# Kernel tuning notes

Measured on AMD Instinct MI355X. Metric: run time of the kernel, lower is better.

The kernel has to match this reference:

```python
import jax, jax.numpy as jnp
import numpy as np
from jax import lax

DIM = 256
PROJ = 128
NPOS = 8          # ceil(log2(2*64+5))
EXT = 64          # attnExtension
NLAYERS = 4
HEADS = 4
KDIM = PROJ + NPOS
EPS = 1e-5


def _ln(x):
    # LayerNorm over last dim, no affine (elementwise_affine=False)
    mu = jnp.mean(x, axis=-1, keepdims=True)
    var = jnp.mean(jnp.square(x - mu), axis=-1, keepdims=True)
    return (x - mu) * lax.rsqrt(var + EPS)


def setup_inputs() -> dict:
    key = jax.random.key(0)
    ks = jax.random.split(key, 18)
    L = 2048
    s = 0.05
    return {
        "input": jax.random.normal(ks[0], (L, PROJ), jnp.float32),
        "residual": jax.random.normal(ks[1], (5 * L, DIM), jnp.float32),
        "W_proj": jax.random.normal(ks[2], (5 * DIM, KDIM), jnp.float32) * s,
        "b_proj": jnp.zeros((5 * DIM,), jnp.float32),
        "Wq": jax.random.normal(ks[3], (DIM, DIM), jnp.float32) * s,
        "bq": jnp.zeros((DIM,), jnp.float32),
        "Wk": jax.random.normal(ks[4], (DIM, KDIM), jnp.float32) * s,
        "bk": jnp.zeros((DIM,), jnp.float32),
        "Wv": jax.random.normal(ks[5], (DIM, KDIM), jnp.float32) * s,
        "bv": jnp.zeros((DIM,), jnp.float32),
        "Wo": jax.random.normal(ks[6], (DIM, DIM), jnp.float32) * s,
        "bo": jnp.zeros((DIM,), jnp.float32),
        "conv_w": jax.random.normal(ks[7], (NLAYERS, DIM, DIM, 3), jnp.float32) * s,
        "conv_b": jnp.zeros((NLAYERS, DIM), jnp.float32),
        "W_skip": jax.random.normal(ks[8], (DIM, DIM), jnp.float32) * s,
        "b_skip": jnp.zeros((DIM,), jnp.float32),
    }


def reference(input, residual, W_proj, b_proj, Wq, bq, Wk, bk, Wv, bv,
              Wo, bo, conv_w, conv_b, W_skip, b_skip):
    L = input.shape[0]
    T = 5 * L  # tgt length
    hd = DIM // HEADS

    # positional embeddings: pos[:, i] = (arange(L) % 2^(i+1)) / 2^i
    n = jnp.arange(L, dtype=input.dtype)[:, None]
    i = jnp.arange(NPOS, dtype=input.dtype)[None, :]
    pos = jnp.mod(n, 2.0 ** (i + 1.0)) / (2.0 ** i)

    src = jnp.concatenate([input, pos], axis=1)            # (L, KDIM)
    tgt = (src @ W_proj.T + b_proj).reshape(T, DIM)        # (5L, DIM)

    # banded mask: row j may attend col i iff 5i-EXT <= j < 5i+5+EXT
    j = jnp.arange(T)[:, None]
    ii = jnp.arange(L)[None, :]
    d = j - 5 * ii
    allowed = (d >= -EXT) & (d < 5 + EXT)                  # (5L, L)

    # multihead attention (eval mode, dropout skipped)
    q = (tgt @ Wq.T + bq).reshape(T, HEADS, hd).transpose(1, 0, 2)
    k = (src @ Wk.T + bk).reshape(L, HEADS, hd).transpose(1, 0, 2)
    v = (src @ Wv.T + bv).reshape(L, HEADS, hd).transpose(1, 0, 2)
    scores = jnp.einsum('hqd,hkd->hqk', q, k) / jnp.sqrt(jnp.asarray(hd, q.dtype))
    scores = jnp.where(allowed[None], scores, -jnp.inf)
    attn = jax.nn.softmax(scores, axis=-1)
    ctx = jnp.einsum('hqk,hkd->hqd', attn, v).transpose(1, 0, 2).reshape(T, DIM)
    attn_out = ctx @ Wo.T + bo

    cnn_in = _ln(attn_out) + residual                      # (5L, DIM)

    # spectral-norm conv stack (weights assumed pre-normalized) + tanh
    x = cnn_in.T[None]                                     # (1, DIM, 5L)
    for l in range(NLAYERS):
        x = jnp.tanh(
            lax.conv_general_dilated(x, conv_w[l], window_strides=(1,),
                                     padding=[(1, 1)])
            + conv_b[l][None, :, None])
    cnn_out = x[0].T                                       # (5L, DIM)

    return _ln(cnn_out + cnn_in @ W_skip.T + b_skip)
```

## Files before the change

### kernel.cpp

```cpp
#include <hip/hip_runtime.h>
#include <hip/hip_bf16.h>

#define PROJ 128
#define KPAD 192
#define EPS 1e-5f
#define CVALID 40

typedef __attribute__((ext_vector_type(4))) float f32x4;
typedef __attribute__((ext_vector_type(8))) short bf16x8;
typedef __attribute__((ext_vector_type(4))) unsigned int u32x4;

__device__ inline float bflo(unsigned u){ union{unsigned x;float f;}c; c.x = u<<16; return c.f; }
__device__ inline float bfhi(unsigned u){ union{unsigned x;float f;}c; c.x = u & 0xffff0000u; return c.f; }
__device__ inline float bf2f(unsigned short u){ union{unsigned x;float f;}c; c.x = ((unsigned)u)<<16; return c.f; }
__device__ inline unsigned short f2bf(float f){
    union{float f; unsigned u;} c; c.f = f;
    unsigned r = c.u + 0x7fff + ((c.u >> 16) & 1);
    return (unsigned short)(r >> 16);
}
__device__ __forceinline__ bf16x8 asbf(u32x4 u){ union{u32x4 a; bf16x8 b;} c; c.a = u; return c.b; }
__device__ __forceinline__ unsigned pk2(float a, float b){
    return (unsigned)f2bf(a) | ((unsigned)f2bf(b) << 16);
}

__global__ __launch_bounds__(256) void prep_all(
    const float* __restrict__ W_proj, const float* __restrict__ Wq,
    const float* __restrict__ Wk, const float* __restrict__ Wv,
    const float* __restrict__ Wo, const float* __restrict__ Ws,
    const float* __restrict__ convw, const float* __restrict__ input,
    const float* __restrict__ bq, const float* __restrict__ b_proj,
    unsigned short* __restrict__ Wqb, unsigned short* __restrict__ Wkb,
    unsigned short* __restrict__ Wvb, unsigned short* __restrict__ Wob,
    unsigned short* __restrict__ Wsb, unsigned short* __restrict__ Wcb,
    unsigned short* __restrict__ WpbT, unsigned short* __restrict__ srcb,
    float* __restrict__ zbias, float* __restrict__ bqc, int L)
{
    int idx = blockIdx.x * 256 + threadIdx.x;
    if (idx < 81920) {
        int w = idx >> 6, lanei = idx & 63;
        int r = w >> 8, o = w & 255;
        const float* wrow = Wq + (size_t)o * 256;
        const float* bp = b_proj + r * 256;
        float s = 0.f;
        #pragma unroll
        for (int c = 0; c < 256; c += 64) s += wrow[c + lanei] * bp[c + lanei];
        #pragma unroll
        for (int m = 32; m > 0; m >>= 1) s += __shfl_xor(s, m, 64);
        if (lanei == 0) bqc[w] = s + bq[o];
        return;
    }
    idx -= 81920;
    if (idx < 8192) {
        const float* s = Wq + (size_t)idx * 8;
        *(u32x4*)&Wqb[(size_t)idx * 8] =
            (u32x4){pk2(s[0],s[1]), pk2(s[2],s[3]), pk2(s[4],s[5]), pk2(s[6],s[7])};
        return;
    }
    idx -= 8192;
    if (idx < 12288) {
        int which = idx / 6144, t = idx % 6144;
        int r = t / 24, c0 = (t % 24) * 8;
        const float* W = which ? Wv : Wk;
        unsigned short* D = which ? Wvb : Wkb;
        u32x4 v = {0,0,0,0};
        if (c0 < 136) {
            const float* s = W + (size_t)r * 136 + c0;
            v = (u32x4){pk2(s[0],s[1]), pk2(s[2],s[3]), pk2(s[4],s[5]), pk2(s[6],s[7])};
        }
        *(u32x4*)&D[(size_t)r * 192 + c0] = v;
        return;
    }
    idx -= 12288;
    if (idx < 16384) {
        int which = idx / 8192, t = idx % 8192;
        int lane = t & 63, fr = (t >> 6) & 3, wid = (t >> 8) & 7, kt = t >> 11;
        int o = wid * 32 + (fr >> 1) * 16 + (lane & 15);
        int c = kt * 64 + (fr & 1) * 32 + (lane >> 4) * 8;
        const float* s = (which ? Ws : Wo) + (size_t)o * 256 + c;
        unsigned short* D = which ? Wsb : Wob;
        *(u32x4*)&D[(size_t)t * 8] =
            (u32x4){pk2(s[0],s[1]), pk2(s[2],s[3]), pk2(s[4],s[5]), pk2(s[6],s[7])};
        return;
    }
    idx -= 16384;
    if (idx < 98304) {
        int t = idx;
        int lane = t & 63, fr = (t >> 6) & 3, wid = (t >> 8) & 7, ktl = t >> 11;
        int l = ktl / 12, kt = ktl % 12;
        int o = wid * 32 + (fr >> 1) * 16 + (lane & 15);
        int c = kt * 64 + (fr & 1) * 32 + (lane >> 4) * 8;
        int ktap = c >> 8, ci = c & 255;
        const float* s = convw + (((size_t)l * 256 + o) * 256 + ci) * 3 + ktap;
        float v[8];
        #pragma unroll
        for (int j = 0; j < 8; ++j) v[j] = s[(size_t)j * 3];
        *(u32x4*)&Wcb[(size_t)t * 8] =
            (u32x4){pk2(v[0],v[1]), pk2(v[2],v[3]), pk2(v[4],v[5]), pk2(v[6],v[7])};
        return;
    }
    idx -= 98304;
    if (idx < 40960) {
        int t = idx;
        int r = t >> 13;
        int c = (t >> 5) & 255;
        int d0 = (t & 31) * 8;
        u32x4 v = {0,0,0,0};
        if (c < 136) {
            const float* s = W_proj + ((size_t)(r * 256 + d0)) * 136 + c;
            float x[8];
            #pragma unroll
            for (int j = 0; j < 8; ++j) x[j] = s[(size_t)j * 136];
            v = (u32x4){pk2(x[0],x[1]), pk2(x[2],x[3]), pk2(x[4],x[5]), pk2(x[6],x[7])};
        }
        *(u32x4*)&WpbT[(size_t)t * 8] = v;
        return;
    }
    idx -= 40960;
    if (idx < L * 24) {
        int n = idx / 24, c0 = (idx % 24) * 8;
        u32x4 v = {0,0,0,0};
        if (c0 < PROJ) {
            const float* s = input + (size_t)n * PROJ + c0;
            v = (u32x4){pk2(s[0],s[1]), pk2(s[2],s[3]), pk2(s[4],s[5]), pk2(s[6],s[7])};
        } else if (c0 == PROJ) {
            float p[8];
            #pragma unroll
            for (int i = 0; i < 8; ++i) {
                int mask = (2 << i) - 1;
                p[i] = (float)(n & mask) / (float)(1 << i);
            }
            v = (u32x4){pk2(p[0],p[1]), pk2(p[2],p[3]), pk2(p[4],p[5]), pk2(p[6],p[7])};
        }
        *(u32x4*)&srcb[(size_t)n * KPAD + c0] = v;
        return;
    }
    idx -= L * 24;
    if (idx < 256) { zbias[idx] = 0.f; return; }
}

__device__ __forceinline__ void gemm_core_64x128(
    unsigned short (&As)[64][72], unsigned short (&Bs)[128][72],
    const unsigned short* __restrict__ A, int lda,
    const unsigned short* __restrict__ B, int ldb,
    const float* __restrict__ bias,
    unsigned short* __restrict__ C, int ldc,
    int K, int m0, int n0)
{
    const int tid = threadIdx.x;
    const int lane = tid & 63;
    const int wid = tid >> 6;
    const int wm = wid >> 1, wn = wid & 1;

    const int ar = tid >> 2, asg = tid & 3;
    const int br = tid >> 1, bsg = tid & 1;

    const unsigned short* Ap = A + (size_t)(m0 + ar) * lda + asg * 16;
    const unsigned short* Bp = B + (size_t)(n0 + br) * ldb + bsg * 32;

    u32x4 ra0, ra1, rb0, rb1, rb2, rb3;
    auto loadregs = [&](int k0) {
        ra0 = *(const u32x4*)(Ap + k0);
        ra1 = *(const u32x4*)(Ap + k0 + 8);
        rb0 = *(const u32x4*)(Bp + k0);
        rb1 = *(const u32x4*)(Bp + k0 + 8);
        rb2 = *(const u32x4*)(Bp + k0 + 16);
        rb3 = *(const u32x4*)(Bp + k0 + 24);
    };
    auto stlds = [&]() {
        *(u32x4*)&As[ar][asg * 16]      = ra0;
        *(u32x4*)&As[ar][asg * 16 + 8]  = ra1;
        *(u32x4*)&Bs[br][bsg * 32]      = rb0;
        *(u32x4*)&Bs[br][bsg * 32 + 8]  = rb1;
        *(u32x4*)&Bs[br][bsg * 32 + 16] = rb2;
        *(u32x4*)&Bs[br][bsg * 32 + 24] = rb3;
    };

    f32x4 acc[2][4];
    #pragma unroll
    for (int i = 0; i < 2; ++i)
        #pragma unroll
        for (int j = 0; j < 4; ++j) acc[i][j] = (f32x4){0.f, 0.f, 0.f, 0.f};

    loadregs(0);
    stlds();
    __syncthreads();

    const int rowf = lane & 15, kb = lane >> 4;
    const int ktiles = K >> 6;
    for (int kt = 0; kt < ktiles; ++kt) {
        if (kt + 1 < ktiles) loadregs((kt + 1) << 6);
        #pragma unroll
        for (int ks = 0; ks < 2; ++ks) {
            bf16x8 af[2], bfr[4];
            #pragma unroll
            for (int i = 0; i < 2; ++i)
                af[i] = *(const bf16x8*)&As[wm * 32 + i * 16 + rowf][ks * 32 + kb * 8];
            #pragma unroll
            for (int j = 0; j < 4; ++j)
                bfr[j] = *(const bf16x8*)&Bs[wn * 64 + j * 16 + rowf][ks * 32 + kb * 8];
            #pragma unroll
            for (int i = 0; i < 2; ++i)
                #pragma unroll
                for (int j = 0; j < 4; ++j)
                    acc[i][j] = __builtin_amdgcn_mfma_f32_16x16x32_bf16(af[i], bfr[j], acc[i][j], 0, 0, 0);
        }
        __syncthreads();
        if (kt + 1 < ktiles) { stlds(); __syncthreads(); }
    }

    const int rq = lane >> 4;
    #pragma unroll
    for (int i = 0; i < 2; ++i) {
        int gm = m0 + wm * 32 + i * 16 + rq * 4;
        #pragma unroll
        for (int j = 0; j < 4; ++j) {
            int gn = n0 + wn * 64 + j * 16 + rowf;
            float bv = bias[gn];
            #pragma unroll
            for (int r = 0; r < 4; ++r)
                C[(size_t)(gm + r) * ldc + gn] = f2bf(acc[i][j][r] + bv);
        }
    }
}

__global__ __launch_bounds__(256) void combine_wq(
    const unsigned short* __restrict__ Wqb,
    const unsigned short* __restrict__ WpbT,
    const float* __restrict__ zbias,
    unsigned short* __restrict__ Wqpb)
{
    __shared__ unsigned short As[64][72];
    __shared__ unsigned short Bs[128][72];
    int bi = blockIdx.x;
    int r = bi >> 3, rem = bi & 7;
    int m0 = (rem >> 1) * 64, n0 = (rem & 1) * 128;
    gemm_core_64x128(As, Bs, Wqb, 256, WpbT + (size_t)r * 65536, 256, zbias,
                     Wqpb + (size_t)r * 65536, 256, 256, m0, n0);
}

__global__ __launch_bounds__(256) void qkv_fused(
    const unsigned short* __restrict__ srcb,
    const unsigned short* __restrict__ Wqpb,
    const unsigned short* __restrict__ Wkb,
    const unsigned short* __restrict__ Wvb,
    const float* __restrict__ bqc, const float* __restrict__ bk,
    const float* __restrict__ bv,
    unsigned short* __restrict__ qb, unsigned short* __restrict__ kb,
    unsigned short* __restrict__ vb)
{
    __shared__ unsigned short As[64][72];
    __shared__ unsigned short Bs[128][72];
    int bi = blockIdx.x;
    const unsigned short *B;
    const float* bias;
    unsigned short* C;
    int ldb, K, m0, n0, ldc;
    if (bi < 320) {
        B = Wqpb; bias = bqc; C = qb; ldb = 256; K = 192; ldc = 1280;
        m0 = (bi / 10) * 64; n0 = (bi % 10) * 128;
    } else if (bi < 384) {
        int t = bi - 320;
        B = Wkb; bias = bk; C = kb; ldb = 192; K = 192; ldc = 256;
        m0 = (t >> 1) * 64; n0 = (t & 1) * 128;
    } else {
        int t = bi - 384;
        B = Wvb; bias = bv; C = vb; ldb = 192; K = 192; ldc = 256;
        m0 = (t >> 1) * 64; n0 = (t & 1) * 128;
    }
    gemm_core_64x128(As, Bs, srcb, KPAD, B, ldb, bias, C, ldc, K, m0, n0);
}

__global__ __launch_bounds__(256) void attn16(
    const unsigned short* __restrict__ q,
    const unsigned short* __restrict__ k,
    const unsigned short* __restrict__ v,
    unsigned short* __restrict__ ctx, int L)
{
    __shared__ unsigned short ksm[30][264];
    __shared__ unsigned short vsm[30][264];
    const int j0 = blockIdx.x * 16;
    const int iblk0 = (j0 >= 68) ? (j0 - 64) / 5 : 0;
    int ihim = (j0 + 79) / 5; if (ihim > L - 1) ihim = L - 1;
    const int NR = ihim - iblk0 + 1;

    for (int e = threadIdx.x; e < 30 * 32; e += 256) {
        int rr = e >> 5, cc = (e & 31) * 8;
        u32x4 kz = {0, 0, 0, 0}, vz = {0, 0, 0, 0};
        if (rr < NR) {
            kz = *(const u32x4*)&k[(size_t)(iblk0 + rr) * 256 + cc];
            vz = *(const u32x4*)&v[(size_t)(iblk0 + rr) * 256 + cc];
        }
        *(u32x4*)&ksm[rr][cc] = kz;
        *(u32x4*)&vsm[rr][cc] = vz;
    }
    __syncthreads();

    const int tid = threadIdx.x;
    const int h = tid >> 6, lane = tid & 63;
    const int qq = lane & 15, p = lane >> 4;
    const int j = j0 + qq;
    const int colb = h * 64 + p * 16;

    float qr[16];
    {
        u32x4 q0 = *(const u32x4*)&q[(size_t)j * 256 + colb];
        u32x4 q1 = *(const u32x4*)&q[(size_t)j * 256 + colb + 8];
        #pragma unroll
        for (int w = 0; w < 4; ++w) {
            qr[2 * w]     = bflo(q0[w]) * 0.125f;
            qr[2 * w + 1] = bfhi(q0[w]) * 0.125f;
            qr[8 + 2 * w]     = bflo(q1[w]) * 0.125f;
            qr[8 + 2 * w + 1] = bfhi(q1[w]) * 0.125f;
        }
    }
    const int ilo = (j >= 68) ? (j - 64) / 5 : 0;
    int ihi = (j + 64) / 5; if (ihi > L - 1) ihi = L - 1;

    float sc[30];
    #pragma unroll
    for (int t = 0; t < 30; ++t) {
        int i = iblk0 + t;
        u32x4 k0 = *(const u32x4*)&ksm[t][colb];
        u32x4 k1 = *(const u32x4*)&ksm[t][colb + 8];
        float s = 0.f;
        #pragma unroll
        for (int w = 0; w < 4; ++w) {
            s += qr[2 * w]     * bflo(k0[w]);
            s += qr[2 * w + 1] * bfhi(k0[w]);
            s += qr[8 + 2 * w]     * bflo(k1[w]);
            s += qr[8 + 2 * w + 1] * bfhi(k1[w]);
        }
        s += __shfl_xor(s, 16, 64);
        s += __shfl_xor(s, 32, 64);
        sc[t] = (i >= ilo && i <= ihi) ? s : -1e30f;
    }
    float mx = -1e30f;
    #pragma unroll
    for (int t = 0; t < 30; ++t) mx = fmaxf(mx, sc[t]);
    float den = 0.f, o[16];
    #pragma unroll
    for (int d = 0; d < 16; ++d) o[d] = 0.f;
    #pragma unroll
    for (int t = 0; t < 30; ++t) {
        float pt = __expf(sc[t] - mx);
        den += pt;
        u32x4 v0 = *(const u32x4*)&vsm[t][colb];
        u32x4 v1 = *(const u32x4*)&vsm[t][colb + 8];
        #pragma unroll
        for (int w = 0; w < 4; ++w) {
            o[2 * w]     += pt * bflo(v0[w]);
            o[2 * w + 1] += pt * bfhi(v0[w]);
            o[8 + 2 * w]     += pt * bflo(v1[w]);
            o[8 + 2 * w + 1] += pt * bfhi(v1[w]);
        }
    }
    float inv = 1.f / den;
    #pragma unroll
    for (int d = 0; d < 16; ++d)
        ctx[(size_t)j * 256 + colb + d] = f2bf(o[d] * inv);
}

__device__ __forceinline__ void wload4a(u32x4 (&b)[4], const unsigned short* p) {
    asm volatile(
        "global_load_dwordx4 %0, %4, off\n\t"
        "global_load_dwordx4 %1, %4, off offset:1024\n\t"
        "global_load_dwordx4 %2, %4, off offset:2048\n\t"
        "global_load_dwordx4 %3, %4, off offset:3072"
        : "=&v"(b[0]), "=&v"(b[1]), "=&v"(b[2]), "=&v"(b[3])
        : "v"(p));
}
__device__ __forceinline__ void wwait8a(u32x4 (&b)[4]) {
    asm volatile("s_waitcnt vmcnt(8)" : "+v"(b[0]), "+v"(b[1]), "+v"(b[2]), "+v"(b[3]));
}
__device__ __forceinline__ void wwait4a(u32x4 (&b)[4]) {
    asm volatile("s_waitcnt vmcnt(4)" : "+v"(b[0]), "+v"(b[1]), "+v"(b[2]), "+v"(b[3]));
}
__device__ __forceinline__ void wwait0a(u32x4 (&b)[4]) {
    asm volatile("s_waitcnt vmcnt(0)" : "+v"(b[0]), "+v"(b[1]), "+v"(b[2]), "+v"(b[3]));
}

template<int NKT, int DTMODE, int NROW>
__device__ __forceinline__ void frag_gemm(
    const unsigned short* __restrict__ Wp,
    const unsigned short (*actin)[264],
    f32x4 (&acc)[NROW][2], int wid, int lane)
{
    const int rowf = lane & 15, kq = lane >> 4;
    const unsigned short* base = Wp + wid * 2048 + lane * 8;
    u32x4 W[3][4];

    wload4a(W[0], base);
    if (NKT > 1) wload4a(W[1], base + 16384);
    if (NKT > 2) wload4a(W[2], base + 2 * 16384);
    if (NKT > 2)      wwait8a(W[0]);
    else if (NKT > 1) wwait4a(W[0]);
    else              wwait0a(W[0]);

    #pragma unroll
    for (int kt = 0; kt < NKT; ++kt) {
        u32x4 (&cur)[4] = W[kt % 3];
        const int dt = (DTMODE == 0) ? (kt >> 2) : (DTMODE == 1 ? 1 : 0);
        const int cb = (DTMODE == 0) ? ((kt & 3) * 64) : (kt * 64);
        #pragma unroll
        for (int ks = 0; ks < 2; ++ks) {
            bf16x8 w0 = asbf(ks ? cur[1] : cur[0]);
            bf16x8 w1 = asbf(ks ? cur[3] : cur[2]);
            #pragma unroll
            for (int i = 0; i < NROW; ++i) {
                bf16x8 a = *(const bf16x8*)&actin[i * 16 + rowf + dt][cb + ks * 32 + kq * 8];
                acc[i][0] = __builtin_amdgcn_mfma_f32_16x16x32_bf16(a, w0, acc[i][0], 0, 0, 0);
                acc[i][1] = __builtin_amdgcn_mfma_f32_16x16x32_bf16(a, w1, acc[i][1], 0, 0, 0);
            }
        }
        if (kt + 3 < NKT) {
            wload4a(cur, base + (size_t)(kt + 3) * 16384);
            wwait8a(W[(kt + 1) % 3]);
        } else if (kt + 2 < NKT) {
            wwait4a(W[(kt + 1) % 3]);
        } else if (kt + 1 < NKT) {
            wwait0a(W[(kt + 1) % 3]);
        }
    }
}

__global__ __launch_bounds__(512)
__attribute__((amdgpu_waves_per_eu(2)))
void conv_mega(
    const unsigned short* __restrict__ ctx,
    const float* __restrict__ residual,
    const unsigned short* __restrict__ Wob,
    const float* __restrict__ bo,
    const unsigned short* __restrict__ Wcb,
    const float* __restrict__ conv_b,
    const unsigned short* __restrict__ Wsb,
    const float* __restrict__ b_skip,
    float* __restrict__ out, int T)
{
    __shared__ unsigned short actA[50][264];
    __shared__ unsigned short actB[64][264];
    __shared__ float redS[64][8];
    __shared__ float redQ[64][8];

    const int tid = threadIdx.x;
    const int lane = tid & 63;
    const int wid = tid >> 6;
    const int rowf = lane & 15;
    const int kq = lane >> 4;
    const int t0 = blockIdx.x * CVALID;
    const int gn0 = wid * 32 + rowf;

    for (int e = tid; e < 64 * 32; e += 512) {
        int b = e >> 5, c = (e & 31) * 8;
        int g = t0 - 5 + b;
        u32x4 z = {0, 0, 0, 0};
        if (g >= 0 && g < T)
            z = *(const u32x4*)&ctx[(size_t)g * 256 + c];
        *(u32x4*)&actB[b][c] = z;
    }
    __syncthreads();

    f32x4 wacc[4][2];
    #pragma unroll
    for (int i = 0; i < 4; ++i)
        #pragma unroll
        for (int j = 0; j < 2; ++j) wacc[i][j] = (f32x4){0.f, 0.f, 0.f, 0.f};
    frag_gemm<4, 2, 4>(Wob, actB, wacc, wid, lane);

    float bo0 = bo[gn0], bo1 = bo[gn0 + 16];
    #pragma unroll
    for (int i = 0; i < 4; ++i)
        #pragma unroll
        for (int r = 0; r < 4; ++r) {
            float a = wacc[i][0][r] + bo0;
            float b = wacc[i][1][r] + bo1;
            wacc[i][0][r] = a; wacc[i][1][r] = b;
            float s = a + b;
            float q = a * a + b * b;
            #pragma unroll
            for (int m = 1; m < 16; m <<= 1) {
                s += __shfl_xor(s, m, 64);
                q += __shfl_xor(q, m, 64);
            }
            if (rowf == 0) {
                int row = i * 16 + kq * 4 + r;
                redS[row][wid] = s;
                redQ[row][wid] = q;
            }
        }
    __syncthreads();

    #pragma unroll
    for (int i = 0; i < 4; ++i)
        #pragma unroll
        for (int r = 0; r < 4; ++r) {
            int row = i * 16 + kq * 4 + r;
            if (row >= 50) continue;
            int g = t0 - 5 + row;
            float s = 0.f, q = 0.f;
            #pragma unroll
            for (int x = 0; x < 8; ++x) { s += redS[row][x]; q += redQ[row][x]; }
            float mu = s * (1.f / 256.f);
            float var = q * (1.f / 256.f) - mu * mu;
            float rs = rsqrtf(var + EPS);
            unsigned short o0 = 0, o1 = 0;
            if (g >= 0 && g < T) {
                o0 = f2bf((wacc[i][0][r] - mu) * rs + residual[(size_t)g * 256 + gn0]);
                o1 = f2bf((wacc[i][1][r] - mu) * rs + residual[(size_t)g * 256 + gn0 + 16]);
            }
            actA[row][gn0]      = o0;
            actA[row][gn0 + 16] = o1;
        }
    __syncthreads();

    f32x4 skipacc[3][2];
    #pragma unroll
    for (int i = 0; i < 3; ++i)
        #pragma unroll
        for (int j = 0; j < 2; ++j) skipacc[i][j] = (f32x4){0.f, 0.f, 0.f, 0.f};
    frag_gemm<4, 1, 3>(Wsb, actA, skipacc, wid, lane);

    f32x4 cacc[3][2];
    #pragma unroll 1
    for (int l2 = 0; l2 < 2; ++l2) {
        const int le = 2 * l2;
        #pragma unroll
        for (int i = 0; i < 3; ++i)
            #pragma unroll
            for (int j = 0; j < 2; ++j) cacc[i][j] = (f32x4){0.f, 0.f, 0.f, 0.f};
        frag_gemm<12, 0, 3>(Wcb + (size_t)le * 196608, actA, cacc, wid, lane);
        {
            float b0 = conv_b[le * 256 + gn0];
            float b1 = conv_b[le * 256 + gn0 + 16];
            #pragma unroll
            for (int i = 0; i < 3; ++i)
                #pragma unroll
                for (int r = 0; r < 4; ++r) {
                    int w = i * 16 + kq * 4 + r;
                    int g = t0 - 4 + w;
                    bool ok = (g >= 0 && g < T);
                    float v0 = cacc[i][0][r] + b0;
                    float v1 = cacc[i][1][r] + b1;
                    v0 = 1.f - 2.f / (__expf(2.f * v0) + 1.f);
                    v1 = 1.f - 2.f / (__expf(2.f * v1) + 1.f);
                    actB[w + 1][gn0]      = ok ? f2bf(v0) : (unsigned short)0;
                    actB[w + 1][gn0 + 16] = ok ? f2bf(v1) : (unsigned short)0;
                }
            if (tid < 256) actB[0][tid] = 0; else actB[49][tid - 256] = 0;
            __syncthreads();
        }

        const int lo = 2 * l2 + 1;
        #pragma unroll
        for (int i = 0; i < 3; ++i)
            #pragma unroll
            for (int j = 0; j < 2; ++j) cacc[i][j] = (f32x4){0.f, 0.f, 0.f, 0.f};
        frag_gemm<12, 0, 3>(Wcb + (size_t)lo * 196608, actB, cacc, wid, lane);
        {
            float b0 = conv_b[lo * 256 + gn0];
            float b1 = conv_b[lo * 256 + gn0 + 16];
            if (l2 == 0) {
                #pragma unroll
                for (int i = 0; i < 3; ++i)
                    #pragma unroll
                    for (int r = 0; r < 4; ++r) {
                        int w = i * 16 + kq * 4 + r;
                        int g = t0 - 4 + w;
                        bool ok = (g >= 0 && g < T);
                        float v0 = cacc[i][0][r] + b0;
                        float v1 = cacc[i][1][r] + b1;
                        v0 = 1.f - 2.f / (__expf(2.f * v0) + 1.f);
                        v1 = 1.f - 2.f / (__expf(2.f * v1) + 1.f);
                        actA[w + 1][gn0]      = ok ? f2bf(v0) : (unsigned short)0;
                        actA[w + 1][gn0 + 16] = ok ? f2bf(v1) : (unsigned short)0;
                    }
                if (tid < 256) actA[0][tid] = 0; else actA[49][tid - 256] = 0;
                __syncthreads();
            } else {
                float sb0 = b_skip[gn0], sb1 = b_skip[gn0 + 16];
                #pragma unroll
                for (int i = 0; i < 3; ++i)
                    #pragma unroll
                    for (int r = 0; r < 4; ++r) {
                        int w = i * 16 + kq * 4 + r;
                        int g = t0 - 4 + w;
                        bool ok = (g >= 0 && g < T);
                        float v0 = cacc[i][0][r] + b0;
                        float v1 = cacc[i][1][r] + b1;
                        v0 = ok ? (1.f - 2.f / (__expf(2.f * v0) + 1.f)) : 0.f;
                        v1 = ok ? (1.f - 2.f / (__expf(2.f * v1) + 1.f)) : 0.f;
                        skipacc[i][0][r] += sb0 + v0;
                        skipacc[i][1][r] += sb1 + v1;
                    }
            }
        }
    }

    #pragma unroll
    for (int i = 0; i < 3; ++i)
        #pragma unroll
        for (int r = 0; r < 4; ++r) {
            float a = skipacc[i][0][r], b = skipacc[i][1][r];
            float s = a + b;
            float q = a * a + b * b;
            #pragma unroll
            for (int m = 1; m < 16; m <<= 1) {
                s += __shfl_xor(s, m, 64);
                q += __shfl_xor(q, m, 64);
            }
            if (rowf == 0) {
                int row = i * 16 + kq * 4 + r;
                redS[row][wid] = s;
                redQ[row][wid] = q;
            }
        }
    __syncthreads();

    #pragma unroll
    for (int i = 0; i < 3; ++i)
        #pragma unroll
        for (int r = 0; r < 4; ++r) {
            int row = i * 16 + kq * 4 + r;
            if (row < 4 || row >= 44) continue;
            int g = t0 - 4 + row;
            if (g >= T) continue;
            float s = 0.f, q = 0.f;
            #pragma unroll
            for (int x = 0; x < 8; ++x) { s += redS[row][x]; q += redQ[row][x]; }
            float mu = s * (1.f / 256.f);
            float var = q * (1.f / 256.f) - mu * mu;
            float rs = rsqrtf(var + EPS);
            out[(size_t)g * 256 + gn0]      = (skipacc[i][0][r] - mu) * rs;
            out[(size_t)g * 256 + gn0 + 16] = (skipacc[i][1][r] - mu) * rs;
        }
}

extern "C" void kernel_launch(void* const* d_in, const int* in_sizes, int n_in,
                              void* d_out, int out_size, void* d_ws, size_t ws_size,
                              hipStream_t stream) {
    const float* input    = (const float*)d_in[0];
    const float* residual = (const float*)d_in[1];
    const float* W_proj   = (const float*)d_in[2];
    const float* b_proj   = (const float*)d_in[3];
    const float* Wq       = (const float*)d_in[4];
    const float* bq       = (const float*)d_in[5];
    const float* Wk       = (const float*)d_in[6];
    const float* bk       = (const float*)d_in[7];
    const float* Wv       = (const float*)d_in[8];
    const float* bv       = (const float*)d_in[9];
    const float* Wo       = (const float*)d_in[10];
    const float* bo       = (const float*)d_in[11];
    const float* conv_w   = (const float*)d_in[12];
    const float* conv_b   = (const float*)d_in[13];
    const float* W_skip   = (const float*)d_in[14];
    const float* b_skip   = (const float*)d_in[15];
    float* out = (float*)d_out;

    const int L = in_sizes[0] / PROJ;
    const int T = 5 * L;

    unsigned short* w16 = (unsigned short*)d_ws;
    size_t off = 0;
    auto alloc = [&](size_t n) { unsigned short* p = w16 + off; off += n; return p; };
    unsigned short* Wqb   = alloc(65536);
    unsigned short* Wkb   = alloc(49152);
    unsigned short* Wvb   = alloc(49152);
    unsigned short* Wob   = alloc(65536);
    unsigned short* Wsb   = alloc(65536);
    unsigned short* Wcb   = alloc(786432);
    unsigned short* WpbT  = alloc(327680);
    unsigned short* Wqpb  = alloc(327680);
    unsigned short* srcb  = alloc((size_t)L * KPAD);
    unsigned short* tgtb  = alloc((size_t)T * 256);
    unsigned short* qb    = alloc((size_t)T * 256);
    unsigned short* kb    = alloc((size_t)L * 256);
    unsigned short* vb    = alloc((size_t)L * 256);
    float* zbias = (float*)alloc(512);
    float* bqc   = (float*)alloc(2560);

    prep_all<<<dim3(1201), 256, 0, stream>>>(
        W_proj, Wq, Wk, Wv, Wo, W_skip, conv_w, input, bq, b_proj,
        Wqb, Wkb, Wvb, Wob, Wsb, Wcb, WpbT, srcb, zbias, bqc, L);

    combine_wq<<<dim3(40), 256, 0, stream>>>(Wqb, WpbT, zbias, Wqpb);

    qkv_fused<<<dim3(448), 256, 0, stream>>>(
        srcb, Wqpb, Wkb, Wvb, bqc, bk, bv, qb, kb, vb);

    attn16<<<dim3(T / 16), 256, 0, stream>>>(qb, kb, vb, tgtb, L);

    conv_mega<<<dim3(T / CVALID), 512, 0, stream>>>(
        tgtb, residual, Wob, bo, Wcb, conv_b, Wsb, b_skip, out, T);
}
```

Measured before the change: 85.16 us.

## Split conv_mega across 16 waves with one 16-column MFMA tile each

The fused conv/skip/LN kernel now launches 1024 threads (16 waves), each owning a single 16-output-column tile instead of two, and the weight pre-packing layout is changed to match. Residual loads and the first Wo weight prefetch are issued before the activation staging barrier so they overlap it, and shared memory moves to dynamic allocation with 16-way reduction buffers. The aim is more latency hiding and MFMA parallelism per block. In exchange, each wave re-reads the activation fragments for half as much work, and LDS traffic and register pressure per block rise.

```diff
diff --git a/kernel.cpp b/kernel.cpp
--- a/kernel.cpp
+++ b/kernel.cpp
@@ -73,9 +73,12 @@
     idx -= 12288;
     if (idx < 16384) {
         int which = idx / 8192, t = idx % 8192;
-        int lane = t & 63, fr = (t >> 6) & 3, wid = (t >> 8) & 7, kt = t >> 11;
-        int o = wid * 32 + (fr >> 1) * 16 + (lane & 15);
-        int c = kt * 64 + (fr & 1) * 32 + (lane >> 4) * 8;
+        int lane = t & 63;
+        int ks = (t >> 6) & 1;
+        int wid = (t >> 7) & 15;
+        int kt = t >> 11;
+        int o = wid * 16 + (lane & 15);
+        int c = kt * 64 + ks * 32 + (lane >> 4) * 8;
         const float* s = (which ? Ws : Wo) + (size_t)o * 256 + c;
         unsigned short* D = which ? Wsb : Wob;
         *(u32x4*)&D[(size_t)t * 8] =
@@ -85,10 +88,13 @@
     idx -= 16384;
     if (idx < 98304) {
         int t = idx;
-        int lane = t & 63, fr = (t >> 6) & 3, wid = (t >> 8) & 7, ktl = t >> 11;
+        int lane = t & 63;
+        int ks = (t >> 6) & 1;
+        int wid = (t >> 7) & 15;
+        int ktl = t >> 11;
         int l = ktl / 12, kt = ktl % 12;
-        int o = wid * 32 + (fr >> 1) * 16 + (lane & 15);
-        int c = kt * 64 + (fr & 1) * 32 + (lane >> 4) * 8;
+        int o = wid * 16 + (lane & 15);
+        int c = kt * 64 + ks * 32 + (lane >> 4) * 8;
         int ktap = c >> 8, ci = c & 255;
         const float* s = convw + (((size_t)l * 256 + o) * 256 + ci) * 3 + ktap;
         float v[8];
@@ -360,71 +366,74 @@
         ctx[(size_t)j * 256 + colb + d] = f2bf(o[d] * inv);
 }
 
-__device__ __forceinline__ void wload4a(u32x4 (&b)[4], const unsigned short* p) {
+__device__ __forceinline__ void wload2a(u32x4 (&b)[2], const unsigned short* p) {
     asm volatile(
-        "global_load_dwordx4 %0, %4, off\n\t"
-        "global_load_dwordx4 %1, %4, off offset:1024\n\t"
-        "global_load_dwordx4 %2, %4, off offset:2048\n\t"
-        "global_load_dwordx4 %3, %4, off offset:3072"
-        : "=&v"(b[0]), "=&v"(b[1]), "=&v"(b[2]), "=&v"(b[3])
-        : "v"(p));
-}
-__device__ __forceinline__ void wwait8a(u32x4 (&b)[4]) {
-    asm volatile("s_waitcnt vmcnt(8)" : "+v"(b[0]), "+v"(b[1]), "+v"(b[2]), "+v"(b[3]));
-}
-__device__ __forceinline__ void wwait4a(u32x4 (&b)[4]) {
-    asm volatile("s_waitcnt vmcnt(4)" : "+v"(b[0]), "+v"(b[1]), "+v"(b[2]), "+v"(b[3]));
-}
-__device__ __forceinline__ void wwait0a(u32x4 (&b)[4]) {
-    asm volatile("s_waitcnt vmcnt(0)" : "+v"(b[0]), "+v"(b[1]), "+v"(b[2]), "+v"(b[3]));
+        "global_load_dwordx4 %0, %2, off\n\t"
+        "global_load_dwordx4 %1, %2, off offset:1024"
+        : "=&v"(b[0]), "=&v"(b[1]) : "v"(p));
+}
+__device__ __forceinline__ void w2wait4(u32x4 (&b)[2]) {
+    asm volatile("s_waitcnt vmcnt(4)" : "+v"(b[0]), "+v"(b[1]));
+}
+__device__ __forceinline__ void w2wait2(u32x4 (&b)[2]) {
+    asm volatile("s_waitcnt vmcnt(2)" : "+v"(b[0]), "+v"(b[1]));
+}
+__device__ __forceinline__ void w2wait0(u32x4 (&b)[2]) {
+    asm volatile("s_waitcnt vmcnt(0)" : "+v"(b[0]), "+v"(b[1]));
 }
 
 template<int NKT, int DTMODE, int NROW>
-__device__ __forceinline__ void frag_gemm(
+__device__ __forceinline__ void frag_gemm16_body(
+    const unsigned short* __restrict__ base,
+    const unsigned short (*actin)[264],
+    f32x4 (&acc)[NROW], u32x4 (&W)[3][2], int lane)
+{
+    const int rowf = lane & 15, kq = lane >> 4;
+    if (NKT > 2)      w2wait4(W[0]);
+    else if (NKT > 1) w2wait2(W[0]);
+    else              w2wait0(W[0]);
+
+    #pragma unroll
+    for (int kt = 0; kt < NKT; ++kt) {
+        u32x4 (&cur)[2] = W[kt % 3];
+        const int dt = (DTMODE == 0) ? (kt >> 2) : (DTMODE == 1 ? 1 : 0);
+        const int cb = (DTMODE == 0) ? ((kt & 3) * 64) : (kt * 64);
+        #pragma unroll
+        for (int ks = 0; ks < 2; ++ks) {
+            bf16x8 w = asbf(cur[ks]);
+            #pragma unroll
+            for (int i = 0; i < NROW; ++i) {
+                bf16x8 a = *(const bf16x8*)&actin[i * 16 + rowf + dt][cb + ks * 32 + kq * 8];
+                acc[i] = __builtin_amdgcn_mfma_f32_16x16x32_bf16(a, w, acc[i], 0, 0, 0);
+            }
+        }
+        if (kt + 3 < NKT) {
+            wload2a(cur, base + (size_t)(kt + 3) * 16384);
+            w2wait4(W[(kt + 1) % 3]);
+        } else if (kt + 2 < NKT) {
+            w2wait2(W[(kt + 1) % 3]);
+        } else if (kt + 1 < NKT) {
+            w2wait0(W[(kt + 1) % 3]);
+        }
+    }
+}
+
+template<int NKT, int DTMODE, int NROW>
+__device__ __forceinline__ void frag_gemm16(
     const unsigned short* __restrict__ Wp,
     const unsigned short (*actin)[264],
-    f32x4 (&acc)[NROW][2], int wid, int lane)
+    f32x4 (&acc)[NROW], int wid, int lane)
 {
-    const int rowf = lane & 15, kq = lane >> 4;
-    const unsigned short* base = Wp + wid * 2048 + lane * 8;
-    u32x4 W[3][4];
-
-    wload4a(W[0], base);
-    if (NKT > 1) wload4a(W[1], base + 16384);
-    if (NKT > 2) wload4a(W[2], base + 2 * 16384);
-    if (NKT > 2)      wwait8a(W[0]);
-    else if (NKT > 1) wwait4a(W[0]);
-    else              wwait0a(W[0]);
-
-    #pragma unroll
-    for (int kt = 0; kt < NKT; ++kt) {
-        u32x4 (&cur)[4] = W[kt % 3];
-        const int dt = (DTMODE == 0) ? (kt >> 2) : (DTMODE == 1 ? 1 : 0);
-        const int cb = (DTMODE == 0) ? ((kt & 3) * 64) : (kt * 64);
-        #pragma unroll
-        for (int ks = 0; ks < 2; ++ks) {
-            bf16x8 w0 = asbf(ks ? cur[1] : cur[0]);
-            bf16x8 w1 = asbf(ks ? cur[3] : cur[2]);
-            #pragma unroll
-            for (int i = 0; i < NROW; ++i) {
-                bf16x8 a = *(const bf16x8*)&actin[i * 16 + rowf + dt][cb + ks * 32 + kq * 8];
-                acc[i][0] = __builtin_amdgcn_mfma_f32_16x16x32_bf16(a, w0, acc[i][0], 0, 0, 0);
-                acc[i][1] = __builtin_amdgcn_mfma_f32_16x16x32_bf16(a, w1, acc[i][1], 0, 0, 0);
-            }
-        }
-        if (kt + 3 < NKT) {
-            wload4a(cur, base + (size_t)(kt + 3) * 16384);
-            wwait8a(W[(kt + 1) % 3]);
-        } else if (kt + 2 < NKT) {
-            wwait4a(W[(kt + 1) % 3]);
-        } else if (kt + 1 < NKT) {
-            wwait0a(W[(kt + 1) % 3]);
-        }
-    }
-}
-
-__global__ __launch_bounds__(512)
-__attribute__((amdgpu_waves_per_eu(2)))
+    const unsigned short* base = Wp + wid * 1024 + lane * 8;
+    u32x4 W[3][2];
+    wload2a(W[0], base);
+    if (NKT > 1) wload2a(W[1], base + 16384);
+    if (NKT > 2) wload2a(W[2], base + 2 * 16384);
+    frag_gemm16_body<NKT, DTMODE, NROW>(base, actin, acc, W, lane);
+}
+
+__global__ __launch_bounds__(1024)
+__attribute__((amdgpu_waves_per_eu(4)))
 void conv_mega(
     const unsigned short* __restrict__ ctx,
     const float* __restrict__ residual,
@@ -436,10 +445,12 @@
     const float* __restrict__ b_skip,
     float* __restrict__ out, int T)
 {
-    __shared__ unsigned short actA[50][264];
-    __shared__ unsigned short actB[64][264];
-    __shared__ float redS[64][8];
-    __shared__ float redQ[64][8];
+    extern __shared__ char smem[];
+    typedef unsigned short u16;
+    u16 (*actA)[264] = (u16(*)[264])smem;
+    u16 (*actB)[264] = (u16(*)[264])(smem + 26400);
+    float (*redS)[16] = (float(*)[16])(smem + 60192);
+    float (*redQ)[16] = (float(*)[16])(smem + 64288);
 
     const int tid = threadIdx.x;
     const int lane = tid & 63;
@@ -447,9 +458,30 @@
     const int rowf = lane & 15;
     const int kq = lane >> 4;
     const int t0 = blockIdx.x * CVALID;
-    const int gn0 = wid * 32 + rowf;
-
-    for (int e = tid; e < 64 * 32; e += 512) {
+    const int gn0 = wid * 16 + rowf;
+
+    float resv[4][4];
+    #pragma unroll
+    for (int i = 0; i < 4; ++i)
+        #pragma unroll
+        for (int r = 0; r < 4; ++r) {
+            int row = i * 16 + kq * 4 + r;
+            int g = t0 - 5 + row;
+            float r0 = 0.f;
+            if (row < 50 && g >= 0 && g < T) {
+                const float* p = residual + (size_t)g * 256 + gn0;
+                asm volatile("global_load_dword %0, %1, off" : "=&v"(r0) : "v"(p));
+            }
+            resv[i][r] = r0;
+        }
+
+    const unsigned short* wbase0 = Wob + wid * 1024 + lane * 8;
+    u32x4 WW[3][2];
+    wload2a(WW[0], wbase0);
+    wload2a(WW[1], wbase0 + 16384);
+    wload2a(WW[2], wbase0 + 2 * 16384);
+
+    for (int e = tid; e < 64 * 32; e += 1024) {
         int b = e >> 5, c = (e & 31) * 8;
         int g = t0 - 5 + b;
         u32x4 z = {0, 0, 0, 0};
@@ -459,23 +491,20 @@
     }
     __syncthreads();
 
-    f32x4 wacc[4][2];
+    f32x4 wacc[4];
+    #pragma unroll
+    for (int i = 0; i < 4; ++i) wacc[i] = (f32x4){0.f, 0.f, 0.f, 0.f};
+    frag_gemm16_body<4, 2, 4>(wbase0, actB, wacc, WW, lane);
+
+    float bo0 = bo[gn0];
     #pragma unroll
     for (int i = 0; i < 4; ++i)
         #pragma unroll
-        for (int j = 0; j < 2; ++j) wacc[i][j] = (f32x4){0.f, 0.f, 0.f, 0.f};
-    frag_gemm<4, 2, 4>(Wob, actB, wacc, wid, lane);
-
-    float bo0 = bo[gn0], bo1 = bo[gn0 + 16];
-    #pragma unroll
-    for (int i = 0; i < 4; ++i)
-        #pragma unroll
         for (int r = 0; r < 4; ++r) {
-            float a = wacc[i][0][r] + bo0;
-            float b = wacc[i][1][r] + bo1;
-            wacc[i][0][r] = a; wacc[i][1][r] = b;
-            float s = a + b;
-            float q = a * a + b * b;
+            float a = wacc[i][r] + bo0;
+            wacc[i][r] = a;
+            float s = a;
+            float q = a * a;
             #pragma unroll
             for (int m = 1; m < 16; m <<= 1) {
                 s += __shfl_xor(s, m, 64);
@@ -489,6 +518,12 @@
         }
     __syncthreads();
 
+    asm volatile("s_waitcnt vmcnt(0)");
+    #pragma unroll
+    for (int i = 0; i < 4; ++i)
+        asm volatile("" : "+v"(resv[i][0]), "+v"(resv[i][1]),
+                          "+v"(resv[i][2]), "+v"(resv[i][3]));
+
     #pragma unroll
     for (int i = 0; i < 4; ++i)
         #pragma unroll
@@ -498,39 +533,31 @@
             int g = t0 - 5 + row;
             float s = 0.f, q = 0.f;
             #pragma unroll
-            for (int x = 0; x < 8; ++x) { s += redS[row][x]; q += redQ[row][x]; }
+            for (int x = 0; x < 16; ++x) { s += redS[row][x]; q += redQ[row][x]; }
             float mu = s * (1.f / 256.f);
             float var = q * (1.f / 256.f) - mu * mu;
             float rs = rsqrtf(var + EPS);
-            unsigned short o0 = 0, o1 = 0;
-            if (g >= 0 && g < T) {
-                o0 = f2bf((wacc[i][0][r] - mu) * rs + residual[(size_t)g * 256 + gn0]);
-                o1 = f2bf((wacc[i][1][r] - mu) * rs + residual[(size_t)g * 256 + gn0 + 16]);
-            }
-            actA[row][gn0]      = o0;
-            actA[row][gn0 + 16] = o1;
+            unsigned short o0 = 0;
+            if (g >= 0 && g < T)
+                o0 = f2bf((wacc[i][r] - mu) * rs + resv[i][r]);
+            actA[row][gn0] = o0;
         }
     __syncthreads();
 
-    f32x4 skipacc[3][2];
-    #pragma unroll
-    for (int i = 0; i < 3; ++i)
-        #pragma unroll
-        for (int j = 0; j < 2; ++j) skipacc[i][j] = (f32x4){0.f, 0.f, 0.f, 0.f};
-    frag_gemm<4, 1, 3>(Wsb, actA, skipacc, wid, lane);
-
-    f32x4 cacc[3][2];
+    f32x4 skipacc[3];
+    #pragma unroll
+    for (int i = 0; i < 3; ++i) skipacc[i] = (f32x4){0.f, 0.f, 0.f, 0.f};
+    frag_gemm16<4, 1, 3>(Wsb, actA, skipacc, wid, lane);
+
+    f32x4 cacc[3];
     #pragma unroll 1
     for (int l2 = 0; l2 < 2; ++l2) {
         const int le = 2 * l2;
         #pragma unroll
-        for (int i = 0; i < 3; ++i)
-            #pragma unroll
-            for (int j = 0; j < 2; ++j) cacc[i][j] = (f32x4){0.f, 0.f, 0.f, 0.f};
-        frag_gemm<12, 0, 3>(Wcb + (size_t)le * 196608, actA, cacc, wid, lane);
+        for (int i = 0; i < 3; ++i) cacc[i] = (f32x4){0.f, 0.f, 0.f, 0.f};
+        frag_gemm16<12, 0, 3>(Wcb + (size_t)le * 196608, actA, cacc, wid, lane);
         {
             float b0 = conv_b[le * 256 + gn0];
-            float b1 = conv_b[le * 256 + gn0 + 16];
             #pragma unroll
             for (int i = 0; i < 3; ++i)
                 #pragma unroll
@@ -538,26 +565,21 @@
                     int w = i * 16 + kq * 4 + r;
                     int g = t0 - 4 + w;
                     bool ok = (g >= 0 && g < T);
-                    float v0 = cacc[i][0][r] + b0;
-                    float v1 = cacc[i][1][r] + b1;
+                    float v0 = cacc[i][r] + b0;
                     v0 = 1.f - 2.f / (__expf(2.f * v0) + 1.f);
-                    v1 = 1.f - 2.f / (__expf(2.f * v1) + 1.f);
-                    actB[w + 1][gn0]      = ok ? f2bf(v0) : (unsigned short)0;
-                    actB[w + 1][gn0 + 16] = ok ? f2bf(v1) : (unsigned short)0;
+                    actB[w + 1][gn0] = ok ? f2bf(v0) : (unsigned short)0;
                 }
-            if (tid < 256) actB[0][tid] = 0; else actB[49][tid - 256] = 0;
+            if (tid < 256) actB[0][tid] = 0;
+            else if (tid < 512) actB[49][tid - 256] = 0;
             __syncthreads();
         }
 
         const int lo = 2 * l2 + 1;
         #pragma unroll
-        for (int i = 0; i < 3; ++i)
-            #pragma unroll
-            for (int j = 0; j < 2; ++j) cacc[i][j] = (f32x4){0.f, 0.f, 0.f, 0.f};
-        frag_gemm<12, 0, 3>(Wcb + (size_t)lo * 196608, actB, cacc, wid, lane);
+        for (int i = 0; i < 3; ++i) cacc[i] = (f32x4){0.f, 0.f, 0.f, 0.f};
+        frag_gemm16<12, 0, 3>(Wcb + (size_t)lo * 196608, actB, cacc, wid, lane);
         {
             float b0 = conv_b[lo * 256 + gn0];
-            float b1 = conv_b[lo * 256 + gn0 + 16];
             if (l2 == 0) {
                 #pragma unroll
                 for (int i = 0; i < 3; ++i)
@@ -566,17 +588,15 @@
                         int w = i * 16 + kq * 4 + r;
                         int g = t0 - 4 + w;
                         bool ok = (g >= 0 && g < T);
-                        float v0 = cacc[i][0][r] + b0;
-                        float v1 = cacc[i][1][r] + b1;
+                        float v0 = cacc[i][r] + b0;
                         v0 = 1.f - 2.f / (__expf(2.f * v0) + 1.f);
-                        v1 = 1.f - 2.f / (__expf(2.f * v1) + 1.f);
-                        actA[w + 1][gn0]      = ok ? f2bf(v0) : (unsigned short)0;
-                        actA[w + 1][gn0 + 16] = ok ? f2bf(v1) : (unsigned short)0;
+                        actA[w + 1][gn0] = ok ? f2bf(v0) : (unsigned short)0;
                     }
-                if (tid < 256) actA[0][tid] = 0; else actA[49][tid - 256] = 0;
+                if (tid < 256) actA[0][tid] = 0;
+                else if (tid < 512) actA[49][tid - 256] = 0;
                 __syncthreads();
             } else {
-                float sb0 = b_skip[gn0], sb1 = b_skip[gn0 + 16];
+                float sb0 = b_skip[gn0];
                 #pragma unroll
                 for (int i = 0; i < 3; ++i)
                     #pragma unroll
@@ -584,12 +604,9 @@
                         int w = i * 16 + kq * 4 + r;
                         int g = t0 - 4 + w;
                         bool ok = (g >= 0 && g < T);
-                        float v0 = cacc[i][0][r] + b0;
-                        float v1 = cacc[i][1][r] + b1;
+                        float v0 = cacc[i][r] + b0;
                         v0 = ok ? (1.f - 2.f / (__expf(2.f * v0) + 1.f)) : 0.f;
-                        v1 = ok ? (1.f - 2.f / (__expf(2.f * v1) + 1.f)) : 0.f;
-                        skipacc[i][0][r] += sb0 + v0;
-                        skipacc[i][1][r] += sb1 + v1;
+                        skipacc[i][r] += sb0 + v0;
                     }
             }
         }
@@ -599,9 +616,9 @@
     for (int i = 0; i < 3; ++i)
         #pragma unroll
         for (int r = 0; r < 4; ++r) {
-            float a = skipacc[i][0][r], b = skipacc[i][1][r];
-            float s = a + b;
-            float q = a * a + b * b;
+            float a = skipacc[i][r];
+            float s = a;
+            float q = a * a;
             #pragma unroll
             for (int m = 1; m < 16; m <<= 1) {
                 s += __shfl_xor(s, m, 64);
@@ -625,12 +642,11 @@
             if (g >= T) continue;
             float s = 0.f, q = 0.f;
             #pragma unroll
-            for (int x = 0; x < 8; ++x) { s += redS[row][x]; q += redQ[row][x]; }
+            for (int x = 0; x < 16; ++x) { s += redS[row][x]; q += redQ[row][x]; }
             float mu = s * (1.f / 256.f);
             float var = q * (1.f / 256.f) - mu * mu;
             float rs = rsqrtf(var + EPS);
-            out[(size_t)g * 256 + gn0]      = (skipacc[i][0][r] - mu) * rs;
-            out[(size_t)g * 256 + gn0 + 16] = (skipacc[i][1][r] - mu) * rs;
+            out[(size_t)g * 256 + gn0] = (skipacc[i][r] - mu) * rs;
         }
 }
 
@@ -688,6 +704,8 @@
 
     attn16<<<dim3(T / 16), 256, 0, stream>>>(qb, kb, vb, tgtb, L);
 
-    conv_mega<<<dim3(T / CVALID), 512, 0, stream>>>(
+    hipFuncSetAttribute((const void*)conv_mega,
+                        hipFuncAttributeMaxDynamicSharedMemorySize, 69632);
+    conv_mega<<<dim3(T / CVALID), 1024, 68384, stream>>>(
         tgtb, residual, Wob, bo, Wcb, conv_b, Wsb, b_skip, out, T);
 }
```

Result: slower. 109.0 us (+28.0%).
